# Kernel tuning notes

Hardware: AMD Instinct MI355X
Metric: run time of the kernel (lower is better)

## Reference

```python
import jax, jax.numpy as jnp
import numpy as np

B, T, H, L = 64, 2048, 256, 16


def setup_inputs() -> dict:
    key = jax.random.key(0)
    ks = jax.random.split(key, 6)
    x = jax.random.normal(ks[0], (B, T, H), dtype=jnp.float32)
    tags = jax.random.randint(ks[1], (B, T), 0, L).astype(jnp.int32)
    mask = jnp.ones((B, T), dtype=bool)  # torchcrf requires mask[:,0] all on
    W = jax.random.normal(ks[2], (L, H), dtype=jnp.float32) * (1.0 / np.sqrt(H))
    b = jnp.zeros((L,), dtype=jnp.float32)
    # torchcrf initializes transitions ~ U(-0.1, 0.1)
    start_transitions = jax.random.uniform(ks[3], (L,), minval=-0.1, maxval=0.1)
    end_transitions = jax.random.uniform(ks[4], (L,), minval=-0.1, maxval=0.1)
    transitions = jax.random.uniform(ks[5], (L, L), minval=-0.1, maxval=0.1)
    return {"x": x, "W": W, "b": b,
            "start_transitions": start_transitions,
            "end_transitions": end_transitions,
            "transitions": transitions,
            "tags": tags, "mask": mask}


def reference(x, W, b, start_transitions, end_transitions, transitions, tags, mask):
    # Emitter: Linear(hidden_dim -> num_labels)
    emissions = jnp.einsum('bth,lh->btl', x, W) + b  # [B,T,L]
    maskf = mask.astype(emissions.dtype)             # [B,T]

    # ---- numerator: score of the gold tag path (vectorized, no scan) ----
    emit_gold = jnp.take_along_axis(emissions, tags[..., None].astype(jnp.int32), axis=2)[..., 0]  # [B,T]
    first_tags = tags[:, 0]
    score = start_transitions[first_tags] + emit_gold[:, 0]
    trans_gold = transitions[tags[:, :-1], tags[:, 1:]]  # [B,T-1]
    score = score + jnp.sum((trans_gold + emit_gold[:, 1:]) * maskf[:, 1:], axis=1)
    seq_ends = jnp.sum(mask.astype(jnp.int32), axis=1) - 1  # index of last valid step
    last_tags = jnp.take_along_axis(tags, seq_ends[:, None], axis=1)[:, 0]
    score = score + end_transitions[last_tags]

    # ---- denominator: forward algorithm (log partition) via lax.scan over time ----
    em_t = jnp.swapaxes(emissions, 0, 1)  # [T,B,L]
    mask_t = jnp.swapaxes(mask, 0, 1)     # [T,B]
    alpha0 = start_transitions[None, :] + em_t[0]  # [B,L]

    def step(alpha, inp):
        em, m = inp  # em: [B,L], m: [B]
        # logsumexp over previous label: alpha[b,i] + transitions[i,j] + em[b,j]
        nxt = jax.nn.logsumexp(alpha[:, :, None] + transitions[None, :, :] + em[:, None, :], axis=1)
        alpha = jnp.where(m[:, None], nxt, alpha)
        return alpha, None

    alphaT, _ = jax.lax.scan(step, alpha0, (em_t[1:], mask_t[1:]))
    denom = jax.nn.logsumexp(alphaT + end_transitions[None, :], axis=1)  # [B]

    llh = score - denom          # log-likelihood per sequence
    return -jnp.mean(llh)        # reduction='mean', nll = -crf(...)
```

## Files before the change

kernel.cpp:

```cpp
#include <hip/hip_runtime.h>
#include <math.h>


#define Bb 64
#define Tt 2048
#define Hh 256
#define Ll 16
#define CHUNK 32
#define NC (Tt / CHUNK)

__global__ __launch_bounds__(256) void k_emis(const float* __restrict__ x,
                                              const float* __restrict__ W,
                                              const float* __restrict__ bias,
                                              float* __restrict__ em) {
  __shared__ float Wl[Ll * Hh];
  __shared__ float bl[Ll];
  int tid = threadIdx.x;
  for (int idx = tid; idx < Ll * Hh; idx += 256) Wl[idx] = W[idx];
  if (tid < Ll) bl[tid] = bias[tid];
  __syncthreads();
  int w = tid >> 6, lane = tid & 63, g = lane >> 2, q = lane & 3;
  int rowbase = blockIdx.x * 256 + w * 64 + g;
  const float4* x4 = (const float4*)x;
  float acc[4][16];
#pragma unroll
  for (int r = 0; r < 4; ++r)
#pragma unroll
    for (int l = 0; l < 16; ++l) acc[r][l] = 0.f;
  size_t rb[4];
#pragma unroll
  for (int r = 0; r < 4; ++r) rb[r] = (size_t)(rowbase + r * 16) * 64 + q;

#pragma unroll 4
  for (int i = 0; i < 16; ++i) {
    float4 xv0 = x4[rb[0] + i * 4];
    float4 xv1 = x4[rb[1] + i * 4];
    float4 xv2 = x4[rb[2] + i * 4];
    float4 xv3 = x4[rb[3] + i * 4];
    const float* wp = Wl + i * 16 + q * 4;
#pragma unroll
    for (int l = 0; l < 16; ++l) {
      float4 wv = *(const float4*)(wp + l * Hh);
      acc[0][l] = fmaf(xv0.x, wv.x, fmaf(xv0.y, wv.y, fmaf(xv0.z, wv.z, fmaf(xv0.w, wv.w, acc[0][l]))));
      acc[1][l] = fmaf(xv1.x, wv.x, fmaf(xv1.y, wv.y, fmaf(xv1.z, wv.z, fmaf(xv1.w, wv.w, acc[1][l]))));
      acc[2][l] = fmaf(xv2.x, wv.x, fmaf(xv2.y, wv.y, fmaf(xv2.z, wv.z, fmaf(xv2.w, wv.w, acc[2][l]))));
      acc[3][l] = fmaf(xv3.x, wv.x, fmaf(xv3.y, wv.y, fmaf(xv3.z, wv.z, fmaf(xv3.w, wv.w, acc[3][l]))));
    }
  }

  bool qb0 = (q & 1) != 0, qb1 = (q & 2) != 0;
  float4 bq = *(const float4*)(bl + q * 4);
  float4* em4 = (float4*)em;
#pragma unroll
  for (int r = 0; r < 4; ++r) {
    float t1[16];
#pragma unroll
    for (int l = 0; l < 16; ++l) t1[l] = __shfl_xor(acc[r][l], 1);
    float r8[8];
#pragma unroll
    for (int k = 0; k < 8; ++k)
      r8[k] = qb0 ? (acc[r][8 + k] + t1[8 + k]) : (acc[r][k] + t1[k]);
    float t2[8];
#pragma unroll
    for (int k = 0; k < 8; ++k) t2[k] = __shfl_xor(r8[k], 2);
    float r4[4];
#pragma unroll
    for (int k = 0; k < 4; ++k)
      r4[k] = qb1 ? (r8[4 + k] + t2[4 + k]) : (r8[k] + t2[k]);
    float4 o = make_float4(r4[0] + bq.x, r4[1] + bq.y, r4[2] + bq.z, r4[3] + bq.w);
    em4[(size_t)(rowbase + r * 16) * 4 + q] = o;
  }
}

__global__ __launch_bounds__(64) void k_chunk(const float* __restrict__ em,
                                              const float* __restrict__ trans,
                                              float* __restrict__ Pout,
                                              float* __restrict__ lscale) {
  int c = blockIdx.x, b = blockIdx.y;
  int lane = threadIdx.x;
  int i = lane >> 2, jg = lane & 3;
  __shared__ float gbuf[CHUNK * 16];

  float4 e[16];
#pragma unroll
  for (int k = 0; k < 16; ++k) {
    float4 t4 = *(const float4*)(trans + k * 16 + jg * 4);
    e[k] = make_float4(expf(t4.x), expf(t4.y), expf(t4.z), expf(t4.w));
  }

  float offpart = 0.f;
  if (lane < CHUNK) {
    int t = c * CHUNK + lane;
    const float4* ep = (const float4*)(em + ((size_t)b * Tt + t) * Ll);
    float4 a0 = ep[0], a1 = ep[1], a2 = ep[2], a3 = ep[3];
    float m = fmaxf(fmaxf(fmaxf(fmaxf(a0.x, a0.y), fmaxf(a0.z, a0.w)),
                          fmaxf(fmaxf(a1.x, a1.y), fmaxf(a1.z, a1.w))),
                    fmaxf(fmaxf(fmaxf(a2.x, a2.y), fmaxf(a2.z, a2.w)),
                          fmaxf(fmaxf(a3.x, a3.y), fmaxf(a3.z, a3.w))));
    float4* gp = (float4*)(gbuf + lane * 16);
    gp[0] = make_float4(expf(a0.x - m), expf(a0.y - m), expf(a0.z - m), expf(a0.w - m));
    gp[1] = make_float4(expf(a1.x - m), expf(a1.y - m), expf(a1.z - m), expf(a1.w - m));
    gp[2] = make_float4(expf(a2.x - m), expf(a2.y - m), expf(a2.z - m), expf(a2.w - m));
    gp[3] = make_float4(expf(a3.x - m), expf(a3.y - m), expf(a3.z - m), expf(a3.w - m));
    offpart = (t >= 1) ? m : 0.f;
  }
#pragma unroll
  for (int msk = 1; msk < 64; msk <<= 1) offpart += __shfl_xor(offpart, msk);
  float off = offpart;
  __syncthreads();

  float4 p = make_float4(i == jg * 4 + 0 ? 1.f : 0.f, i == jg * 4 + 1 ? 1.f : 0.f,
                         i == jg * 4 + 2 ? 1.f : 0.f, i == jg * 4 + 3 ? 1.f : 0.f);
  int srcb = lane & ~3;

  int sbeg = (c == 0) ? 1 : 0;
  for (int s = sbeg; s < CHUNK; ++s) {
    float4 pm0, pm1, pm2, pm3;
    pm0.x = __shfl(p.x, srcb + 0); pm0.y = __shfl(p.y, srcb + 0);
    pm0.z = __shfl(p.z, srcb + 0); pm0.w = __shfl(p.w, srcb + 0);
    pm1.x = __shfl(p.x, srcb + 1); pm1.y = __shfl(p.y, srcb + 1);
    pm1.z = __shfl(p.z, srcb + 1); pm1.w = __shfl(p.w, srcb + 1);
    pm2.x = __shfl(p.x, srcb + 2); pm2.y = __shfl(p.y, srcb + 2);
    pm2.z = __shfl(p.z, srcb + 2); pm2.w = __shfl(p.w, srcb + 2);
    pm3.x = __shfl(p.x, srcb + 3); pm3.y = __shfl(p.y, srcb + 3);
    pm3.z = __shfl(p.z, srcb + 3); pm3.w = __shfl(p.w, srcb + 3);
    float4 acc = make_float4(0.f, 0.f, 0.f, 0.f);
#define K4ACC(pmv, kb)                                                              \
    acc.x = fmaf(pmv.x, e[kb + 0].x, acc.x); acc.y = fmaf(pmv.x, e[kb + 0].y, acc.y); \
    acc.z = fmaf(pmv.x, e[kb + 0].z, acc.z); acc.w = fmaf(pmv.x, e[kb + 0].w, acc.w); \
    acc.x = fmaf(pmv.y, e[kb + 1].x, acc.x); acc.y = fmaf(pmv.y, e[kb + 1].y, acc.y); \
    acc.z = fmaf(pmv.y, e[kb + 1].z, acc.z); acc.w = fmaf(pmv.y, e[kb + 1].w, acc.w); \
    acc.x = fmaf(pmv.z, e[kb + 2].x, acc.x); acc.y = fmaf(pmv.z, e[kb + 2].y, acc.y); \
    acc.z = fmaf(pmv.z, e[kb + 2].z, acc.z); acc.w = fmaf(pmv.z, e[kb + 2].w, acc.w); \
    acc.x = fmaf(pmv.w, e[kb + 3].x, acc.x); acc.y = fmaf(pmv.w, e[kb + 3].y, acc.y); \
    acc.z = fmaf(pmv.w, e[kb + 3].z, acc.z); acc.w = fmaf(pmv.w, e[kb + 3].w, acc.w);
    K4ACC(pm0, 0) K4ACC(pm1, 4) K4ACC(pm2, 8) K4ACC(pm3, 12)
#undef K4ACC
    float4 g4 = *(const float4*)(gbuf + s * 16 + jg * 4);
    p.x = acc.x * g4.x; p.y = acc.y * g4.y; p.z = acc.z * g4.z; p.w = acc.w * g4.w;
    if (((s & 7) == 7) || (s == CHUNK - 1)) {
      float mx = fmaxf(fmaxf(p.x, p.y), fmaxf(p.z, p.w));
#pragma unroll
      for (int msk = 1; msk < 64; msk <<= 1) mx = fmaxf(mx, __shfl_xor(mx, msk));
      float inv = __builtin_amdgcn_rcpf(mx);
      p.x *= inv; p.y *= inv; p.z *= inv; p.w *= inv;
      off += logf(mx);
    }
  }
  ((float4*)(Pout + ((size_t)(b * NC + c)) * 256))[lane] = p;
  if (lane == 0) lscale[b * NC + c] = off;
}

__global__ __launch_bounds__(256) void k_gold(const float* __restrict__ em,
                                              const int* __restrict__ tags,
                                              const float* __restrict__ strans,
                                              const float* __restrict__ etrans,
                                              const float* __restrict__ trans,
                                              float* __restrict__ score) {
  int b = blockIdx.x, tid = threadIdx.x;
  const int* tg = tags + (size_t)b * Tt;
  const float* eb = em + (size_t)b * Tt * Ll;
  float s = 0.f;
  for (int t = tid; t < Tt; t += 256) {
    int tag = tg[t];
    if (t == 0) {
      s += strans[tag] + eb[tag];
    } else {
      s += trans[tg[t - 1] * 16 + tag] + eb[(size_t)t * Ll + tag];
    }
  }
  if (tid == 0) s += etrans[tg[Tt - 1]];
  __shared__ float red[256];
  red[tid] = s;
  __syncthreads();
  for (int st = 128; st > 0; st >>= 1) {
    if (tid < st) red[tid] += red[tid + st];
    __syncthreads();
  }
  if (tid == 0) score[b] = red[0];
}

__global__ __launch_bounds__(64) void k_combine(const float* __restrict__ em,
                                                const float* __restrict__ P,
                                                const float* __restrict__ lscale,
                                                const float* __restrict__ strans,
                                                const float* __restrict__ etrans,
                                                float* __restrict__ denom) {
  int b = blockIdx.x, lane = threadIdx.x;
  __shared__ float Pl[NC * 256];
  const float4* src = (const float4*)(P + (size_t)b * NC * 256);
  float4* dst = (float4*)Pl;
  for (int idx = lane; idx < NC * 64; idx += 64) dst[idx] = src[idx];
  float ls = lscale[b * NC + lane];
#pragma unroll
  for (int m = 1; m < 64; m <<= 1) ls += __shfl_xor(ls, m);

  int j = lane & 15, ig = lane >> 4;
  float a = strans[j] + em[(size_t)b * Tt * Ll + j];
  float m0 = a;
#pragma unroll
  for (int m = 1; m < 16; m <<= 1) m0 = fmaxf(m0, __shfl_xor(m0, m));
  float v = expf(a - m0);
  float o = m0 + ls;
  __syncthreads();

  for (int cc = 0; cc < NC; ++cc) {
    const float* Pc = Pl + cc * 256;
    float part = 0.f;
#pragma unroll
    for (int r = 0; r < 4; ++r) {
      int srcl = (ig << 4) + ig * 4 + r;
      float vr = __shfl(v, srcl);
      part = fmaf(vr, Pc[(ig * 4 + r) * 16 + j], part);
    }
    part += __shfl_xor(part, 16);
    part += __shfl_xor(part, 32);
    if ((cc & 3) == 3) {
      float mx = part;
#pragma unroll
      for (int m = 1; m < 16; m <<= 1) mx = fmaxf(mx, __shfl_xor(mx, m));
      o += logf(mx);
      v = part * __builtin_amdgcn_rcpf(mx);
    } else {
      v = part;
    }
  }
  float sj = v * expf(etrans[j]);
#pragma unroll
  for (int m = 1; m < 16; m <<= 1) sj += __shfl_xor(sj, m);
  if (lane == 0) denom[b] = o + logf(sj);
}

__global__ __launch_bounds__(64) void k_final(const float* __restrict__ score,
                                              const float* __restrict__ denom,
                                              float* __restrict__ out) {
  int lane = threadIdx.x;
  float llh = score[lane] - denom[lane];
#pragma unroll
  for (int m = 1; m < 64; m <<= 1) llh += __shfl_xor(llh, m);
  if (lane == 0) out[0] = -llh * (1.0f / 64.0f);
}

extern "C" void kernel_launch(void* const* d_in, const int* in_sizes, int n_in,
                              void* d_out, int out_size, void* d_ws, size_t ws_size,
                              hipStream_t stream) {
  const float* x = (const float*)d_in[0];
  const float* W = (const float*)d_in[1];
  const float* bias = (const float*)d_in[2];
  const float* strans = (const float*)d_in[3];
  const float* etrans = (const float*)d_in[4];
  const float* trans = (const float*)d_in[5];
  const int* tags = (const int*)d_in[6];

  float* ws = (float*)d_ws;
  float* em = ws;
  float* P = em + (size_t)Bb * Tt * Ll;
  float* lscale = P + (size_t)Bb * NC * 256;
  float* score = lscale + (size_t)Bb * NC;
  float* denom = score + Bb;
  float* out = (float*)d_out;

  hipLaunchKernelGGL(k_emis, dim3(Bb * Tt / 256), dim3(256), 0, stream, x, W, bias, em);
  hipLaunchKernelGGL(k_chunk, dim3(NC, Bb), dim3(64), 0, stream, em, trans, P, lscale);
  hipLaunchKernelGGL(k_gold, dim3(Bb), dim3(256), 0, stream, em, tags, strans, etrans, trans, score);
  hipLaunchKernelGGL(k_combine, dim3(Bb), dim3(64), 0, stream, em, P, lscale, strans, etrans, denom);
  hipLaunchKernelGGL(k_final, dim3(1), dim3(64), 0, stream, score, denom, out);
}
```

Baseline: 285.3 us.

## Fuse emission GEMM, gold-path score and chunk scans into one kernel

Merges the emission projection, gold-path scoring and per-chunk forward-algorithm matrix products into a single kernel. Each block keeps its 256-row emission tile in shared memory, so the full [B,T,L] emission tensor is never written to or read back from global memory. Only the first timestep's emissions are saved, for use by the combine kernel. Gold scores are accumulated with atomics after a memset, and the W shared buffer is reused for the exponentiated emissions. The cost is higher shared-memory use per block and a serial chunk scan that runs inside the GEMM blocks, which may lower occupancy.

```diff
diff --git a/kernel.cpp b/kernel.cpp
--- a/kernel.cpp
+++ b/kernel.cpp
@@ -8,179 +8,185 @@
 #define Ll 16
 #define CHUNK 32
 #define NC (Tt / CHUNK)
-
-__global__ __launch_bounds__(256) void k_emis(const float* __restrict__ x,
-                                              const float* __restrict__ W,
-                                              const float* __restrict__ bias,
-                                              float* __restrict__ em) {
+#define ROWS 256
+#define NCHK (ROWS / CHUNK)
+
+__global__ __launch_bounds__(256) void k_fused(const float* __restrict__ x,
+                                               const float* __restrict__ W,
+                                               const float* __restrict__ bias,
+                                               const float* __restrict__ strans,
+                                               const float* __restrict__ etrans,
+                                               const float* __restrict__ trans,
+                                               const int* __restrict__ tags,
+                                               float* __restrict__ em0,
+                                               float* __restrict__ Pout,
+                                               float* __restrict__ lscale,
+                                               float* __restrict__ score) {
   __shared__ float Wl[Ll * Hh];
+  __shared__ float tile[ROWS * Ll];
+  __shared__ float trl[256];
+  __shared__ float etl[256];
+  __shared__ float mbuf[ROWS];
   __shared__ float bl[Ll];
+  __shared__ float red[256];
+  float* ghat = Wl;
+
   int tid = threadIdx.x;
+  int b = blockIdx.x >> 3;
+  int t0 = (blockIdx.x & 7) * ROWS;
+
   for (int idx = tid; idx < Ll * Hh; idx += 256) Wl[idx] = W[idx];
+  trl[tid] = trans[tid];
+  etl[tid] = expf(trl[tid]);
   if (tid < Ll) bl[tid] = bias[tid];
   __syncthreads();
-  int w = tid >> 6, lane = tid & 63, g = lane >> 2, q = lane & 3;
-  int rowbase = blockIdx.x * 256 + w * 64 + g;
-  const float4* x4 = (const float4*)x;
-  float acc[4][16];
-#pragma unroll
-  for (int r = 0; r < 4; ++r)
-#pragma unroll
-    for (int l = 0; l < 16; ++l) acc[r][l] = 0.f;
-  size_t rb[4];
-#pragma unroll
-  for (int r = 0; r < 4; ++r) rb[r] = (size_t)(rowbase + r * 16) * 64 + q;
+
+  {
+    int w = tid >> 6, lane = tid & 63, g = lane >> 2, q = lane & 3;
+    int rowl = w * 64 + g;
+    size_t rowg = (size_t)blockIdx.x * ROWS + rowl;
+    const float4* x4 = (const float4*)x;
+    float acc[4][16];
+#pragma unroll
+    for (int r = 0; r < 4; ++r)
+#pragma unroll
+      for (int l = 0; l < 16; ++l) acc[r][l] = 0.f;
+    size_t rb[4];
+#pragma unroll
+    for (int r = 0; r < 4; ++r) rb[r] = (rowg + (size_t)r * 16) * 64 + q;
 
 #pragma unroll 4
-  for (int i = 0; i < 16; ++i) {
-    float4 xv0 = x4[rb[0] + i * 4];
-    float4 xv1 = x4[rb[1] + i * 4];
-    float4 xv2 = x4[rb[2] + i * 4];
-    float4 xv3 = x4[rb[3] + i * 4];
-    const float* wp = Wl + i * 16 + q * 4;
-#pragma unroll
-    for (int l = 0; l < 16; ++l) {
-      float4 wv = *(const float4*)(wp + l * Hh);
-      acc[0][l] = fmaf(xv0.x, wv.x, fmaf(xv0.y, wv.y, fmaf(xv0.z, wv.z, fmaf(xv0.w, wv.w, acc[0][l]))));
-      acc[1][l] = fmaf(xv1.x, wv.x, fmaf(xv1.y, wv.y, fmaf(xv1.z, wv.z, fmaf(xv1.w, wv.w, acc[1][l]))));
-      acc[2][l] = fmaf(xv2.x, wv.x, fmaf(xv2.y, wv.y, fmaf(xv2.z, wv.z, fmaf(xv2.w, wv.w, acc[2][l]))));
-      acc[3][l] = fmaf(xv3.x, wv.x, fmaf(xv3.y, wv.y, fmaf(xv3.z, wv.z, fmaf(xv3.w, wv.w, acc[3][l]))));
-    }
-  }
-
-  bool qb0 = (q & 1) != 0, qb1 = (q & 2) != 0;
-  float4 bq = *(const float4*)(bl + q * 4);
-  float4* em4 = (float4*)em;
-#pragma unroll
-  for (int r = 0; r < 4; ++r) {
-    float t1[16];
-#pragma unroll
-    for (int l = 0; l < 16; ++l) t1[l] = __shfl_xor(acc[r][l], 1);
-    float r8[8];
-#pragma unroll
-    for (int k = 0; k < 8; ++k)
-      r8[k] = qb0 ? (acc[r][8 + k] + t1[8 + k]) : (acc[r][k] + t1[k]);
-    float t2[8];
-#pragma unroll
-    for (int k = 0; k < 8; ++k) t2[k] = __shfl_xor(r8[k], 2);
-    float r4[4];
-#pragma unroll
-    for (int k = 0; k < 4; ++k)
-      r4[k] = qb1 ? (r8[4 + k] + t2[4 + k]) : (r8[k] + t2[k]);
-    float4 o = make_float4(r4[0] + bq.x, r4[1] + bq.y, r4[2] + bq.z, r4[3] + bq.w);
-    em4[(size_t)(rowbase + r * 16) * 4 + q] = o;
-  }
-}
-
-__global__ __launch_bounds__(64) void k_chunk(const float* __restrict__ em,
-                                              const float* __restrict__ trans,
-                                              float* __restrict__ Pout,
-                                              float* __restrict__ lscale) {
-  int c = blockIdx.x, b = blockIdx.y;
-  int lane = threadIdx.x;
-  int i = lane >> 2, jg = lane & 3;
-  __shared__ float gbuf[CHUNK * 16];
-
-  float4 e[16];
-#pragma unroll
-  for (int k = 0; k < 16; ++k) {
-    float4 t4 = *(const float4*)(trans + k * 16 + jg * 4);
-    e[k] = make_float4(expf(t4.x), expf(t4.y), expf(t4.z), expf(t4.w));
-  }
-
-  float offpart = 0.f;
-  if (lane < CHUNK) {
-    int t = c * CHUNK + lane;
-    const float4* ep = (const float4*)(em + ((size_t)b * Tt + t) * Ll);
-    float4 a0 = ep[0], a1 = ep[1], a2 = ep[2], a3 = ep[3];
+    for (int i = 0; i < 16; ++i) {
+      float4 xv0 = x4[rb[0] + i * 4];
+      float4 xv1 = x4[rb[1] + i * 4];
+      float4 xv2 = x4[rb[2] + i * 4];
+      float4 xv3 = x4[rb[3] + i * 4];
+      const float* wp = Wl + i * 16 + q * 4;
+#pragma unroll
+      for (int l = 0; l < 16; ++l) {
+        float4 wv = *(const float4*)(wp + l * Hh);
+        acc[0][l] = fmaf(xv0.x, wv.x, fmaf(xv0.y, wv.y, fmaf(xv0.z, wv.z, fmaf(xv0.w, wv.w, acc[0][l]))));
+        acc[1][l] = fmaf(xv1.x, wv.x, fmaf(xv1.y, wv.y, fmaf(xv1.z, wv.z, fmaf(xv1.w, wv.w, acc[1][l]))));
+        acc[2][l] = fmaf(xv2.x, wv.x, fmaf(xv2.y, wv.y, fmaf(xv2.z, wv.z, fmaf(xv2.w, wv.w, acc[2][l]))));
+        acc[3][l] = fmaf(xv3.x, wv.x, fmaf(xv3.y, wv.y, fmaf(xv3.z, wv.z, fmaf(xv3.w, wv.w, acc[3][l]))));
+      }
+    }
+    bool qb0 = (q & 1) != 0, qb1 = (q & 2) != 0;
+    float4 bq = *(const float4*)(bl + q * 4);
+#pragma unroll
+    for (int r = 0; r < 4; ++r) {
+      float t1[16];
+#pragma unroll
+      for (int l = 0; l < 16; ++l) t1[l] = __shfl_xor(acc[r][l], 1);
+      float r8[8];
+#pragma unroll
+      for (int k = 0; k < 8; ++k) r8[k] = qb0 ? (acc[r][8 + k] + t1[8 + k]) : (acc[r][k] + t1[k]);
+      float t2[8];
+#pragma unroll
+      for (int k = 0; k < 8; ++k) t2[k] = __shfl_xor(r8[k], 2);
+      float r4[4];
+#pragma unroll
+      for (int k = 0; k < 4; ++k) r4[k] = qb1 ? (r8[4 + k] + t2[4 + k]) : (r8[k] + t2[k]);
+      float4 o = make_float4(r4[0] + bq.x, r4[1] + bq.y, r4[2] + bq.z, r4[3] + bq.w);
+      *(float4*)(tile + (rowl + r * 16) * 16 + q * 4) = o;
+      if (t0 == 0 && r == 0 && tid < 4)
+        *(float4*)(em0 + b * 16 + q * 4) = o;
+    }
+  }
+  __syncthreads();
+
+  {
+    int gt = blockIdx.x * ROWS + tid;
+    int tag = tags[gt];
+    float s;
+    if ((gt & (Tt - 1)) == 0) {
+      s = strans[tag] + tile[tid * 16 + tag];
+    } else {
+      int pv = tags[gt - 1];
+      s = trl[pv * 16 + tag] + tile[tid * 16 + tag];
+    }
+    if ((gt & (Tt - 1)) == (Tt - 1)) s += etrans[tag];
+    red[tid] = s;
+    __syncthreads();
+    for (int st = 128; st > 0; st >>= 1) {
+      if (tid < st) red[tid] += red[tid + st];
+      __syncthreads();
+    }
+    if (tid == 0) atomicAdd(score + b, red[0]);
+  }
+
+  {
+    const float4* tp = (const float4*)(tile + tid * 16);
+    float4 a0 = tp[0], a1 = tp[1], a2 = tp[2], a3 = tp[3];
     float m = fmaxf(fmaxf(fmaxf(fmaxf(a0.x, a0.y), fmaxf(a0.z, a0.w)),
                           fmaxf(fmaxf(a1.x, a1.y), fmaxf(a1.z, a1.w))),
                     fmaxf(fmaxf(fmaxf(a2.x, a2.y), fmaxf(a2.z, a2.w)),
                           fmaxf(fmaxf(a3.x, a3.y), fmaxf(a3.z, a3.w))));
-    float4* gp = (float4*)(gbuf + lane * 16);
+    float4* gp = (float4*)(ghat + tid * 16);
     gp[0] = make_float4(expf(a0.x - m), expf(a0.y - m), expf(a0.z - m), expf(a0.w - m));
     gp[1] = make_float4(expf(a1.x - m), expf(a1.y - m), expf(a1.z - m), expf(a1.w - m));
     gp[2] = make_float4(expf(a2.x - m), expf(a2.y - m), expf(a2.z - m), expf(a2.w - m));
     gp[3] = make_float4(expf(a3.x - m), expf(a3.y - m), expf(a3.z - m), expf(a3.w - m));
-    offpart = (t >= 1) ? m : 0.f;
-  }
-#pragma unroll
-  for (int msk = 1; msk < 64; msk <<= 1) offpart += __shfl_xor(offpart, msk);
-  float off = offpart;
-  __syncthreads();
-
-  float4 p = make_float4(i == jg * 4 + 0 ? 1.f : 0.f, i == jg * 4 + 1 ? 1.f : 0.f,
-                         i == jg * 4 + 2 ? 1.f : 0.f, i == jg * 4 + 3 ? 1.f : 0.f);
-  int srcb = lane & ~3;
-
-  int sbeg = (c == 0) ? 1 : 0;
-  for (int s = sbeg; s < CHUNK; ++s) {
-    float4 pm0, pm1, pm2, pm3;
-    pm0.x = __shfl(p.x, srcb + 0); pm0.y = __shfl(p.y, srcb + 0);
-    pm0.z = __shfl(p.z, srcb + 0); pm0.w = __shfl(p.w, srcb + 0);
-    pm1.x = __shfl(p.x, srcb + 1); pm1.y = __shfl(p.y, srcb + 1);
-    pm1.z = __shfl(p.z, srcb + 1); pm1.w = __shfl(p.w, srcb + 1);
-    pm2.x = __shfl(p.x, srcb + 2); pm2.y = __shfl(p.y, srcb + 2);
-    pm2.z = __shfl(p.z, srcb + 2); pm2.w = __shfl(p.w, srcb + 2);
-    pm3.x = __shfl(p.x, srcb + 3); pm3.y = __shfl(p.y, srcb + 3);
-    pm3.z = __shfl(p.z, srcb + 3); pm3.w = __shfl(p.w, srcb + 3);
-    float4 acc = make_float4(0.f, 0.f, 0.f, 0.f);
-#define K4ACC(pmv, kb)                                                              \
-    acc.x = fmaf(pmv.x, e[kb + 0].x, acc.x); acc.y = fmaf(pmv.x, e[kb + 0].y, acc.y); \
-    acc.z = fmaf(pmv.x, e[kb + 0].z, acc.z); acc.w = fmaf(pmv.x, e[kb + 0].w, acc.w); \
-    acc.x = fmaf(pmv.y, e[kb + 1].x, acc.x); acc.y = fmaf(pmv.y, e[kb + 1].y, acc.y); \
-    acc.z = fmaf(pmv.y, e[kb + 1].z, acc.z); acc.w = fmaf(pmv.y, e[kb + 1].w, acc.w); \
-    acc.x = fmaf(pmv.z, e[kb + 2].x, acc.x); acc.y = fmaf(pmv.z, e[kb + 2].y, acc.y); \
-    acc.z = fmaf(pmv.z, e[kb + 2].z, acc.z); acc.w = fmaf(pmv.z, e[kb + 2].w, acc.w); \
-    acc.x = fmaf(pmv.w, e[kb + 3].x, acc.x); acc.y = fmaf(pmv.w, e[kb + 3].y, acc.y); \
-    acc.z = fmaf(pmv.w, e[kb + 3].z, acc.z); acc.w = fmaf(pmv.w, e[kb + 3].w, acc.w);
-    K4ACC(pm0, 0) K4ACC(pm1, 4) K4ACC(pm2, 8) K4ACC(pm3, 12)
+    mbuf[tid] = m;
+  }
+  __syncthreads();
+
+  {
+    int w = tid >> 6, lane = tid & 63;
+    int i = lane >> 2, jg = lane & 3;
+    int srcb = lane & ~3;
+    float4 e[16];
+#pragma unroll
+    for (int k = 0; k < 16; ++k) e[k] = *(const float4*)(etl + k * 16 + jg * 4);
+
+    for (int cc = 0; cc < 2; ++cc) {
+      int ci = w + cc * 4;
+      int gc = (blockIdx.x & 7) * NCHK + ci;
+      int sbeg = (gc == 0) ? 1 : 0;
+      float off = 0.f;
+      for (int s = sbeg; s < CHUNK; ++s) off += mbuf[ci * CHUNK + s];
+      float4 p = make_float4(i == jg * 4 + 0 ? 1.f : 0.f, i == jg * 4 + 1 ? 1.f : 0.f,
+                             i == jg * 4 + 2 ? 1.f : 0.f, i == jg * 4 + 3 ? 1.f : 0.f);
+      for (int s = sbeg; s < CHUNK; ++s) {
+        float4 pm0, pm1, pm2, pm3;
+        pm0.x = __shfl(p.x, srcb + 0); pm0.y = __shfl(p.y, srcb + 0);
+        pm0.z = __shfl(p.z, srcb + 0); pm0.w = __shfl(p.w, srcb + 0);
+        pm1.x = __shfl(p.x, srcb + 1); pm1.y = __shfl(p.y, srcb + 1);
+        pm1.z = __shfl(p.z, srcb + 1); pm1.w = __shfl(p.w, srcb + 1);
+        pm2.x = __shfl(p.x, srcb + 2); pm2.y = __shfl(p.y, srcb + 2);
+        pm2.z = __shfl(p.z, srcb + 2); pm2.w = __shfl(p.w, srcb + 2);
+        pm3.x = __shfl(p.x, srcb + 3); pm3.y = __shfl(p.y, srcb + 3);
+        pm3.z = __shfl(p.z, srcb + 3); pm3.w = __shfl(p.w, srcb + 3);
+        float4 acc = make_float4(0.f, 0.f, 0.f, 0.f);
+#define K4ACC(pmv, kb)                                                                \
+        acc.x = fmaf(pmv.x, e[kb + 0].x, acc.x); acc.y = fmaf(pmv.x, e[kb + 0].y, acc.y); \
+        acc.z = fmaf(pmv.x, e[kb + 0].z, acc.z); acc.w = fmaf(pmv.x, e[kb + 0].w, acc.w); \
+        acc.x = fmaf(pmv.y, e[kb + 1].x, acc.x); acc.y = fmaf(pmv.y, e[kb + 1].y, acc.y); \
+        acc.z = fmaf(pmv.y, e[kb + 1].z, acc.z); acc.w = fmaf(pmv.y, e[kb + 1].w, acc.w); \
+        acc.x = fmaf(pmv.z, e[kb + 2].x, acc.x); acc.y = fmaf(pmv.z, e[kb + 2].y, acc.y); \
+        acc.z = fmaf(pmv.z, e[kb + 2].z, acc.z); acc.w = fmaf(pmv.z, e[kb + 2].w, acc.w); \
+        acc.x = fmaf(pmv.w, e[kb + 3].x, acc.x); acc.y = fmaf(pmv.w, e[kb + 3].y, acc.y); \
+        acc.z = fmaf(pmv.w, e[kb + 3].z, acc.z); acc.w = fmaf(pmv.w, e[kb + 3].w, acc.w);
+        K4ACC(pm0, 0) K4ACC(pm1, 4) K4ACC(pm2, 8) K4ACC(pm3, 12)
 #undef K4ACC
-    float4 g4 = *(const float4*)(gbuf + s * 16 + jg * 4);
-    p.x = acc.x * g4.x; p.y = acc.y * g4.y; p.z = acc.z * g4.z; p.w = acc.w * g4.w;
-    if (((s & 7) == 7) || (s == CHUNK - 1)) {
-      float mx = fmaxf(fmaxf(p.x, p.y), fmaxf(p.z, p.w));
-#pragma unroll
-      for (int msk = 1; msk < 64; msk <<= 1) mx = fmaxf(mx, __shfl_xor(mx, msk));
-      float inv = __builtin_amdgcn_rcpf(mx);
-      p.x *= inv; p.y *= inv; p.z *= inv; p.w *= inv;
-      off += logf(mx);
-    }
-  }
-  ((float4*)(Pout + ((size_t)(b * NC + c)) * 256))[lane] = p;
-  if (lane == 0) lscale[b * NC + c] = off;
-}
-
-__global__ __launch_bounds__(256) void k_gold(const float* __restrict__ em,
-                                              const int* __restrict__ tags,
-                                              const float* __restrict__ strans,
-                                              const float* __restrict__ etrans,
-                                              const float* __restrict__ trans,
-                                              float* __restrict__ score) {
-  int b = blockIdx.x, tid = threadIdx.x;
-  const int* tg = tags + (size_t)b * Tt;
-  const float* eb = em + (size_t)b * Tt * Ll;
-  float s = 0.f;
-  for (int t = tid; t < Tt; t += 256) {
-    int tag = tg[t];
-    if (t == 0) {
-      s += strans[tag] + eb[tag];
-    } else {
-      s += trans[tg[t - 1] * 16 + tag] + eb[(size_t)t * Ll + tag];
-    }
-  }
-  if (tid == 0) s += etrans[tg[Tt - 1]];
-  __shared__ float red[256];
-  red[tid] = s;
-  __syncthreads();
-  for (int st = 128; st > 0; st >>= 1) {
-    if (tid < st) red[tid] += red[tid + st];
-    __syncthreads();
-  }
-  if (tid == 0) score[b] = red[0];
-}
-
-__global__ __launch_bounds__(64) void k_combine(const float* __restrict__ em,
+        float4 g4 = *(const float4*)(ghat + (ci * CHUNK + s) * 16 + jg * 4);
+        p.x = acc.x * g4.x; p.y = acc.y * g4.y; p.z = acc.z * g4.z; p.w = acc.w * g4.w;
+        if (((s & 7) == 7) || (s == CHUNK - 1)) {
+          float mx = fmaxf(fmaxf(p.x, p.y), fmaxf(p.z, p.w));
+#pragma unroll
+          for (int msk = 1; msk < 64; msk <<= 1) mx = fmaxf(mx, __shfl_xor(mx, msk));
+          float inv = __builtin_amdgcn_rcpf(mx);
+          p.x *= inv; p.y *= inv; p.z *= inv; p.w *= inv;
+          off += logf(mx);
+        }
+      }
+      ((float4*)(Pout + ((size_t)(b * NC + gc)) * 256))[lane] = p;
+      if (lane == 0) lscale[b * NC + gc] = off;
+    }
+  }
+}
+
+__global__ __launch_bounds__(64) void k_combine(const float* __restrict__ em0,
                                                 const float* __restrict__ P,
                                                 const float* __restrict__ lscale,
                                                 const float* __restrict__ strans,
@@ -196,7 +202,7 @@
   for (int m = 1; m < 64; m <<= 1) ls += __shfl_xor(ls, m);
 
   int j = lane & 15, ig = lane >> 4;
-  float a = strans[j] + em[(size_t)b * Tt * Ll + j];
+  float a = strans[j] + em0[b * 16 + j];
   float m0 = a;
 #pragma unroll
   for (int m = 1; m < 16; m <<= 1) m0 = fmaxf(m0, __shfl_xor(m0, m));
@@ -253,16 +259,16 @@
   const int* tags = (const int*)d_in[6];
 
   float* ws = (float*)d_ws;
-  float* em = ws;
-  float* P = em + (size_t)Bb * Tt * Ll;
+  float* em0 = ws;
+  float* P = em0 + Bb * 16;
   float* lscale = P + (size_t)Bb * NC * 256;
-  float* score = lscale + (size_t)Bb * NC;
+  float* score = lscale + Bb * NC;
   float* denom = score + Bb;
   float* out = (float*)d_out;
 
-  hipLaunchKernelGGL(k_emis, dim3(Bb * Tt / 256), dim3(256), 0, stream, x, W, bias, em);
-  hipLaunchKernelGGL(k_chunk, dim3(NC, Bb), dim3(64), 0, stream, em, trans, P, lscale);
-  hipLaunchKernelGGL(k_gold, dim3(Bb), dim3(256), 0, stream, em, tags, strans, etrans, trans, score);
-  hipLaunchKernelGGL(k_combine, dim3(Bb), dim3(64), 0, stream, em, P, lscale, strans, etrans, denom);
+  hipMemsetAsync(score, 0, Bb * sizeof(float), stream);
+  hipLaunchKernelGGL(k_fused, dim3(Bb * Tt / ROWS), dim3(256), 0, stream,
+                     x, W, bias, strans, etrans, trans, tags, em0, P, lscale, score);
+  hipLaunchKernelGGL(k_combine, dim3(Bb), dim3(64), 0, stream, em0, P, lscale, strans, etrans, denom);
   hipLaunchKernelGGL(k_final, dim3(1), dim3(64), 0, stream, score, denom, out);
 }
```

After: 274.0 us. -3.9%, faster.
